# Kernel tuning notes

Hardware: AMD Instinct MI355X
Metric: run time of the kernel (lower is better)

The kernel has to match this reference:

```python
import jax, jax.numpy as jnp
import numpy as np

D_MODEL = 1024
NUM_HEADS = 16
D_HEAD = D_MODEL // NUM_HEADS
MAX_DISTANCE = 128
SEQ_LEN = 2048


def setup_inputs() -> dict:
    key = jax.random.key(0)
    k_x, k_qkv, k_out, k_bias = jax.random.split(key, 4)
    scale = 1.0 / np.sqrt(D_MODEL)
    return {
        "x": jax.random.normal(k_x, (SEQ_LEN, D_MODEL), dtype=jnp.float32),
        "w_qkv": jax.random.normal(k_qkv, (D_MODEL, 3 * D_MODEL), dtype=jnp.float32) * scale,
        "w_out": jax.random.normal(k_out, (D_MODEL, D_MODEL), dtype=jnp.float32) * scale,
        "rel_bias": jax.random.normal(k_bias, (MAX_DISTANCE, NUM_HEADS), dtype=jnp.float32) * 0.02,
    }


def _position_bias(rel_bias, seq_len):
    # relative_position[q, k] = k - q; bucket = clip(|rel|, 0, max_distance-1)
    ctx = jnp.arange(seq_len)[:, None]
    mem = jnp.arange(seq_len)[None, :]
    bucket = jnp.clip(jnp.abs(mem - ctx), 0, MAX_DISTANCE - 1)  # [q, k]
    return rel_bias[bucket]  # [q, k, h]


def reference(x, w_qkv, w_out, rel_bias):
    seq_len = x.shape[0]
    qkv = x @ w_qkv  # [s, 3*d_model]
    q, k, v = jnp.split(qkv, 3, axis=-1)
    q = q.reshape(seq_len, NUM_HEADS, D_HEAD)
    k = k.reshape(seq_len, NUM_HEADS, D_HEAD)
    v = v.reshape(seq_len, NUM_HEADS, D_HEAD)
    bias = _position_bias(rel_bias, seq_len)  # [q, k, h]
    # flax dot_product_attention semantics: scale q by 1/sqrt(d_head), add bias, softmax over kv
    scores = jnp.einsum("qhd,khd->hqk", q, k) / jnp.sqrt(jnp.asarray(D_HEAD, q.dtype))
    scores = scores + jnp.transpose(bias, (2, 0, 1))  # [h, q, k]
    weights = jax.nn.softmax(scores, axis=-1)
    attn = jnp.einsum("hqk,khd->qhd", weights, v)  # [s, h, d_head]
    attn = attn.reshape(1, seq_len, D_MODEL)
    return attn @ w_out  # [1, s, d_model]
```

## Files before the change

### kernel.cpp

```cpp
#include <hip/hip_runtime.h>
#include <hip/hip_bf16.h>

#define SEQ   2048
#define DM    1024
#define NH    16
#define DH    64
#define MAXD  128

typedef __attribute__((ext_vector_type(8))) short  short8;
typedef __attribute__((ext_vector_type(4))) float  float4v;

__device__ __forceinline__ short8 ld8(const void* p) {
    short8 v; __builtin_memcpy(&v, p, 16); return v;
}
__device__ __forceinline__ void st8(void* p, short8 v) {
    __builtin_memcpy(p, &v, 16);
}
__device__ __forceinline__ short bf16bits(float f) {
    __hip_bfloat16 b = __float2bfloat16(f);
    short s; __builtin_memcpy(&s, &b, 2); return s;
}
__device__ __forceinline__ float bits2f(short s) {
    unsigned u = (unsigned)(unsigned short)s << 16;
    return __builtin_bit_cast(float, u);
}

__device__ __forceinline__ void async16(void* lds, const void* g) {
    __builtin_amdgcn_global_load_lds(
        (const __attribute__((address_space(1))) unsigned int*)g,
        (__attribute__((address_space(3))) unsigned int*)lds, 16, 0, 0);
}

template <int CTRL>
__device__ __forceinline__ float dppmov(float x) {
    return __builtin_bit_cast(float,
        __builtin_amdgcn_update_dpp(0, __builtin_bit_cast(int, x), CTRL, 0xf, 0xf, true));
}
__device__ __forceinline__ float red16max(float x) {
    x = fmaxf(x, dppmov<0xB1>(x));
    x = fmaxf(x, dppmov<0x4E>(x));
    x = fmaxf(x, dppmov<0x141>(x));
    x = fmaxf(x, dppmov<0x140>(x));
    return x;
}
__device__ __forceinline__ float red16sum(float x) {
    x += dppmov<0xB1>(x);
    x += dppmov<0x4E>(x);
    x += dppmov<0x141>(x);
    x += dppmov<0x140>(x);
    return x;
}

__global__ __launch_bounds__(256) void cvt_f32_bf16(
    const float* __restrict__ src, __hip_bfloat16* __restrict__ dst) {
    const size_t i = ((size_t)blockIdx.x * 256 + threadIdx.x) * 8;
    float f[8]; __builtin_memcpy(f, src + i, 32);
    short8 v;
#pragma unroll
    for (int j = 0; j < 8; ++j) v[j] = bf16bits(f[j]);
    st8(dst + i, v);
}

__global__ __launch_bounds__(256) void transpose_weights(
    const float* __restrict__ wq, const float* __restrict__ wo,
    __hip_bfloat16* __restrict__ wqT, __hip_bfloat16* __restrict__ woT) {
    __shared__ __hip_bfloat16 tile[32][33];
    const int t = threadIdx.x;
    const int tx = t % 32, ty = t / 32;
    const int bx = blockIdx.x, r0 = blockIdx.y * 32;
    const float* src; __hip_bfloat16* dst; int ss, ds, c0;
    if (bx < 96) { src = wq; dst = wqT; ss = 3 * DM; ds = DM; c0 = bx * 32; }
    else         { src = wo; dst = woT; ss = DM;     ds = DM; c0 = (bx - 96) * 32; }
#pragma unroll
    for (int i = 0; i < 4; ++i)
        tile[ty + i * 8][tx] = __float2bfloat16(src[(size_t)(r0 + ty + i * 8) * ss + c0 + tx]);
    __syncthreads();
#pragma unroll
    for (int i = 0; i < 4; ++i)
        dst[(size_t)(c0 + ty + i * 8) * ds + r0 + tx] = tile[tx][ty + i * 8];
}

__global__ __launch_bounds__(256) void transpose_v(
    const __hip_bfloat16* __restrict__ src, __hip_bfloat16* __restrict__ dst,
    int s_stride, int d_stride) {
    __shared__ __hip_bfloat16 tile[32][33];
    const int t = threadIdx.x;
    const int tx = t % 32, ty = t / 32;
    const int c0 = blockIdx.x * 32, r0 = blockIdx.y * 32;
#pragma unroll
    for (int i = 0; i < 4; ++i)
        tile[ty + i * 8][tx] = src[(size_t)(r0 + ty + i * 8) * s_stride + c0 + tx];
    __syncthreads();
#pragma unroll
    for (int i = 0; i < 4; ++i)
        dst[(size_t)(c0 + ty + i * 8) * d_stride + r0 + tx] = tile[tx][ty + i * 8];
}

template <int NT, typename TC>
__global__ __launch_bounds__(256) void gemm_mfma(
    const __hip_bfloat16* __restrict__ A,
    const __hip_bfloat16* __restrict__ BT,
    TC* __restrict__ C,
    int M, int N, int K) {
    __shared__ short As[128 * 32];
    __shared__ short Bs[32 * NT * 32];

    const int t = threadIdx.x;
    const int w = t >> 6, lane = t & 63;
    const int l15 = lane & 15, quad = lane >> 4;
    const int row0 = blockIdx.y * 128;
    const int col0 = blockIdx.x * (32 * NT);
    const int wm = w >> 1, wn = w & 1;

    float4v acc[4][NT];
#pragma unroll
    for (int i = 0; i < 4; ++i)
#pragma unroll
        for (int j = 0; j < NT; ++j) acc[i][j] = (float4v){0.f, 0.f, 0.f, 0.f};

    const int mloc0 = lane >> 2;
    const int u     = lane & 3;

    for (int k0 = 0; k0 < K; k0 += 32) {
#pragma unroll
        for (int i = 0; i < 2; ++i) {
            const int c = 2 * w + i;
            async16(&As[c * 512], A + (size_t)(row0 + c * 16 + mloc0) * K + k0 + u * 8);
        }
#pragma unroll
        for (int i = 0; i < NT / 2; ++i) {
            const int c = (NT / 2) * w + i;
            async16(&Bs[c * 512], BT + (size_t)(col0 + c * 16 + mloc0) * K + k0 + u * 8);
        }
        __syncthreads();

        short8 af[4], bf[NT];
#pragma unroll
        for (int mt = 0; mt < 4; ++mt)
            af[mt] = ld8(&As[(wm * 64 + mt * 16 + l15) * 32 + quad * 8]);
#pragma unroll
        for (int nt = 0; nt < NT; ++nt)
            bf[nt] = ld8(&Bs[(wn * 16 * NT + nt * 16 + l15) * 32 + quad * 8]);
#pragma unroll
        for (int mt = 0; mt < 4; ++mt)
#pragma unroll
            for (int nt = 0; nt < NT; ++nt)
                acc[mt][nt] = __builtin_amdgcn_mfma_f32_16x16x32_bf16(
                    af[mt], bf[nt], acc[mt][nt], 0, 0, 0);
        __syncthreads();
    }

#pragma unroll
    for (int mt = 0; mt < 4; ++mt)
#pragma unroll
        for (int nt = 0; nt < NT; ++nt)
#pragma unroll
            for (int r = 0; r < 4; ++r) {
                const int row = row0 + wm * 64 + mt * 16 + quad * 4 + r;
                const int col = col0 + wn * 16 * NT + nt * 16 + l15;
                float v = acc[mt][nt][r];
                if constexpr (__is_same(TC, float)) C[(size_t)row * N + col] = v;
                else C[(size_t)row * N + col] = __float2bfloat16(v);
            }
}

#define TK  128
#define KS  68
#define VS  136

__global__ __launch_bounds__(256) void attn_mfma(
    const __hip_bfloat16* __restrict__ qkv,
    const __hip_bfloat16* __restrict__ vT,
    const float* __restrict__ rel_bias,
    __hip_bfloat16* __restrict__ attnb) {
    __shared__ short Kt[TK * KS];
    __shared__ short Vt[DH * VS];
    __shared__ short Pl[4 * 16 * VS];
    __shared__ float biasL[MAXD];

    const int t = threadIdx.x;
    const int w = t >> 6, lane = t & 63;
    const int l15 = lane & 15, quad = lane >> 4;
    const int h  = blockIdx.y;
    const int q0 = blockIdx.x * 64;
    const int qw = q0 + w * 16;

    if (t < MAXD) biasL[t] = rel_bias[t * NH + h];

    short8 qf[2];
#pragma unroll
    for (int c = 0; c < 2; ++c) {
        short8 raw = ld8(qkv + (size_t)(qw + l15) * (3 * DM) + h * DH + c * 32 + quad * 8);
#pragma unroll
        for (int j = 0; j < 8; ++j) qf[c][j] = bf16bits(bits2f(raw[j]) * 0.125f);
    }

    float4v o_acc[4];
#pragma unroll
    for (int nt = 0; nt < 4; ++nt) o_acc[nt] = (float4v){0.f, 0.f, 0.f, 0.f};
    float m_i[4], l_i[4];
#pragma unroll
    for (int r = 0; r < 4; ++r) { m_i[r] = -1e30f; l_i[r] = 0.f; }

    for (int kb = 0; kb < SEQ / TK; ++kb) {
        const int k0 = kb * TK;
#pragma unroll
        for (int p = 0; p < 4; ++p) {
            const int idx = p * 256 + t;
            const int row = idx >> 3, u = idx & 7;
            st8(&Kt[row * KS + u * 8],
                ld8(qkv + (size_t)(k0 + row) * (3 * DM) + DM + h * DH + u * 8));
        }
#pragma unroll
        for (int p = 0; p < 4; ++p) {
            const int idx = p * 256 + t;
            const int row = idx >> 4, u = idx & 15;
            st8(&Vt[row * VS + u * 8],
                ld8(vT + (size_t)(h * DH + row) * SEQ + k0 + u * 8));
        }
        __syncthreads();

        float4v s_acc[8];
#pragma unroll
        for (int kt = 0; kt < 8; ++kt) s_acc[kt] = (float4v){0.f, 0.f, 0.f, 0.f};
#pragma unroll
        for (int c = 0; c < 2; ++c)
#pragma unroll
            for (int kt = 0; kt < 8; ++kt) {
                short8 kf = ld8(&Kt[(kt * 16 + l15) * KS + (c * 4 + quad) * 8]);
                s_acc[kt] = __builtin_amdgcn_mfma_f32_16x16x32_bf16(qf[c], kf, s_acc[kt], 0, 0, 0);
            }

        float sv[8][4];
        const int dlo = k0 - (qw + 15);
        const int dhi = qw - (k0 + TK - 1);
        if (dlo >= MAXD - 1 || dhi >= MAXD - 1) {
            const float bu = biasL[MAXD - 1];
#pragma unroll
            for (int kt = 0; kt < 8; ++kt)
#pragma unroll
                for (int r = 0; r < 4; ++r) sv[kt][r] = s_acc[kt][r] + bu;
        } else {
#pragma unroll
            for (int kt = 0; kt < 8; ++kt)
#pragma unroll
                for (int r = 0; r < 4; ++r) {
                    const int kg = k0 + kt * 16 + l15;
                    const int qg = qw + quad * 4 + r;
                    int rel = kg - qg; if (rel < 0) rel = -rel;
                    if (rel > MAXD - 1) rel = MAXD - 1;
                    sv[kt][r] = s_acc[kt][r] + biasL[rel];
                }
        }

        float rowm[4];
#pragma unroll
        for (int r = 0; r < 4; ++r) {
            float m = sv[0][r];
#pragma unroll
            for (int kt = 1; kt < 8; ++kt) m = fmaxf(m, sv[kt][r]);
            rowm[r] = red16max(m);
        }

        float al[4], rs[4];
#pragma unroll
        for (int r = 0; r < 4; ++r) {
            const float mn = fmaxf(m_i[r], rowm[r]);
            al[r] = __expf(m_i[r] - mn);
            m_i[r] = mn;
            rs[r] = 0.f;
        }
#pragma unroll
        for (int kt = 0; kt < 8; ++kt)
#pragma unroll
            for (int r = 0; r < 4; ++r) {
                const float p = __expf(sv[kt][r] - m_i[r]);
                sv[kt][r] = p;
                rs[r] += p;
            }
#pragma unroll
        for (int r = 0; r < 4; ++r) {
            rs[r] = red16sum(rs[r]);
            l_i[r] = l_i[r] * al[r] + rs[r];
        }
#pragma unroll
        for (int nt = 0; nt < 4; ++nt)
#pragma unroll
            for (int r = 0; r < 4; ++r) o_acc[nt][r] *= al[r];

#pragma unroll
        for (int kt = 0; kt < 8; ++kt)
#pragma unroll
            for (int r = 0; r < 4; ++r)
                Pl[w * 16 * VS + (quad * 4 + r) * VS + kt * 16 + l15] = bf16bits(sv[kt][r]);

#pragma unroll
        for (int kc = 0; kc < 4; ++kc) {
            short8 pf = ld8(&Pl[w * 16 * VS + l15 * VS + kc * 32 + quad * 8]);
#pragma unroll
            for (int nt = 0; nt < 4; ++nt) {
                short8 vf = ld8(&Vt[(nt * 16 + l15) * VS + kc * 32 + quad * 8]);
                o_acc[nt] = __builtin_amdgcn_mfma_f32_16x16x32_bf16(pf, vf, o_acc[nt], 0, 0, 0);
            }
        }
        __syncthreads();
    }

#pragma unroll
    for (int nt = 0; nt < 4; ++nt)
#pragma unroll
        for (int r = 0; r < 4; ++r) {
            const int row = qw + quad * 4 + r;
            const int col = h * DH + nt * 16 + l15;
            attnb[(size_t)row * DM + col] = __float2bfloat16(o_acc[nt][r] / l_i[r]);
        }
}

extern "C" void kernel_launch(void* const* d_in, const int* in_sizes, int n_in,
                              void* d_out, int out_size, void* d_ws, size_t ws_size,
                              hipStream_t stream) {
    const float* x        = (const float*)d_in[0];
    const float* w_qkv    = (const float*)d_in[1];
    const float* w_out    = (const float*)d_in[2];
    const float* rel_bias = (const float*)d_in[3];
    float* out = (float*)d_out;

    char* p = (char*)d_ws;
    __hip_bfloat16* xb    = (__hip_bfloat16*)p;  p += (size_t)SEQ * DM * 2;
    __hip_bfloat16* wqT   = (__hip_bfloat16*)p;  p += (size_t)3 * DM * DM * 2;
    __hip_bfloat16* woT   = (__hip_bfloat16*)p;  p += (size_t)DM * DM * 2;
    __hip_bfloat16* qkvb  = (__hip_bfloat16*)p;  p += (size_t)SEQ * 3 * DM * 2;
    __hip_bfloat16* vT    = (__hip_bfloat16*)p;  p += (size_t)DM * SEQ * 2;
    __hip_bfloat16* attnb = (__hip_bfloat16*)p;

    cvt_f32_bf16<<<SEQ * DM / (256 * 8), 256, 0, stream>>>(x, xb);

    transpose_weights<<<dim3(128, 32), 256, 0, stream>>>(w_qkv, w_out, wqT, woT);

    gemm_mfma<4, __hip_bfloat16><<<dim3(3 * DM / 128, SEQ / 128), 256, 0, stream>>>(
        xb, wqT, qkvb, SEQ, 3 * DM, DM);

    transpose_v<<<dim3(DM / 32, SEQ / 32), 256, 0, stream>>>(
        qkvb + 2 * DM, vT, 3 * DM, SEQ);

    attn_mfma<<<dim3(SEQ / 64, NH), 256, 0, stream>>>(qkvb, vT, rel_bias, attnb);

    gemm_mfma<2, float><<<dim3(DM / 64, SEQ / 128), 256, 0, stream>>>(
        attnb, woT, out, SEQ, DM, DM);
}
```

Measured before the change: 177.7 us.

## Merge prep kernels, shrink GEMM tiles, add 64x64 output GEMM, tweak V padding

Folds the x-to-bf16 conversion into the weight-transpose kernel as extra blocks, which removes one launch. Halves the QKV GEMM column tile so more blocks are launched. Adds a dedicated 64x64-tile GEMM for the output projection so that launch also has more blocks. Changes the V LDS stride padding from 136 to 132. Smaller tiles give more parallelism across CUs but less data reuse per block, and the new stride can change LDS bank conflicts.

```diff
diff --git a/kernel.cpp b/kernel.cpp
--- a/kernel.cpp
+++ b/kernel.cpp
@@ -51,23 +51,26 @@
     return x;
 }
 
-__global__ __launch_bounds__(256) void cvt_f32_bf16(
-    const float* __restrict__ src, __hip_bfloat16* __restrict__ dst) {
-    const size_t i = ((size_t)blockIdx.x * 256 + threadIdx.x) * 8;
-    float f[8]; __builtin_memcpy(f, src + i, 32);
-    short8 v;
-#pragma unroll
-    for (int j = 0; j < 8; ++j) v[j] = bf16bits(f[j]);
-    st8(dst + i, v);
-}
-
-__global__ __launch_bounds__(256) void transpose_weights(
+__global__ __launch_bounds__(256) void prep_kernel(
     const float* __restrict__ wq, const float* __restrict__ wo,
-    __hip_bfloat16* __restrict__ wqT, __hip_bfloat16* __restrict__ woT) {
+    const float* __restrict__ x,
+    __hip_bfloat16* __restrict__ wqT, __hip_bfloat16* __restrict__ woT,
+    __hip_bfloat16* __restrict__ xb) {
+    const int t = threadIdx.x;
+    const int bx = blockIdx.x;
+    if (bx >= 128) {
+        const size_t id = (size_t)(bx - 128) * 32 + blockIdx.y;
+        const size_t i  = id * 2048 + t * 8;
+        float f[8]; __builtin_memcpy(f, x + i, 32);
+        short8 v;
+#pragma unroll
+        for (int j = 0; j < 8; ++j) v[j] = bf16bits(f[j]);
+        st8(xb + i, v);
+        return;
+    }
     __shared__ __hip_bfloat16 tile[32][33];
-    const int t = threadIdx.x;
     const int tx = t % 32, ty = t / 32;
-    const int bx = blockIdx.x, r0 = blockIdx.y * 32;
+    const int r0 = blockIdx.y * 32;
     const float* src; __hip_bfloat16* dst; int ss, ds, c0;
     if (bx < 96) { src = wq; dst = wqT; ss = 3 * DM; ds = DM; c0 = bx * 32; }
     else         { src = wo; dst = woT; ss = DM;     ds = DM; c0 = (bx - 96) * 32; }
@@ -164,9 +167,66 @@
             }
 }
 
+__global__ __launch_bounds__(256) void gemm64(
+    const __hip_bfloat16* __restrict__ A,
+    const __hip_bfloat16* __restrict__ BT,
+    float* __restrict__ C,
+    int M, int N, int K) {
+    __shared__ short As[64 * 32];
+    __shared__ short Bs[64 * 32];
+
+    const int t = threadIdx.x;
+    const int w = t >> 6, lane = t & 63;
+    const int l15 = lane & 15, quad = lane >> 4;
+    const int row0 = blockIdx.y * 64;
+    const int col0 = blockIdx.x * 64;
+    const int wm = w >> 1, wn = w & 1;
+
+    float4v acc[2][2];
+#pragma unroll
+    for (int i = 0; i < 2; ++i)
+#pragma unroll
+        for (int j = 0; j < 2; ++j) acc[i][j] = (float4v){0.f, 0.f, 0.f, 0.f};
+
+    const int mloc0 = lane >> 2;
+    const int u     = lane & 3;
+
+    for (int k0 = 0; k0 < K; k0 += 32) {
+        async16(&As[w * 512], A  + (size_t)(row0 + w * 16 + mloc0) * K + k0 + u * 8);
+        async16(&Bs[w * 512], BT + (size_t)(col0 + w * 16 + mloc0) * K + k0 + u * 8);
+        __syncthreads();
+
+        short8 af[2], bf[2];
+#pragma unroll
+        for (int mt = 0; mt < 2; ++mt)
+            af[mt] = ld8(&As[(wm * 32 + mt * 16 + l15) * 32 + quad * 8]);
+#pragma unroll
+        for (int nt = 0; nt < 2; ++nt)
+            bf[nt] = ld8(&Bs[(wn * 32 + nt * 16 + l15) * 32 + quad * 8]);
+#pragma unroll
+        for (int mt = 0; mt < 2; ++mt)
+#pragma unroll
+            for (int nt = 0; nt < 2; ++nt)
+                acc[mt][nt] = __builtin_amdgcn_mfma_f32_16x16x32_bf16(
+                    af[mt], bf[nt], acc[mt][nt], 0, 0, 0);
+        __syncthreads();
+    }
+
+#pragma unroll
+    for (int mt = 0; mt < 2; ++mt)
+#pragma unroll
+        for (int nt = 0; nt < 2; ++nt)
+#pragma unroll
+            for (int r = 0; r < 4; ++r) {
+                const int row = row0 + wm * 32 + mt * 16 + quad * 4 + r;
+                const int col = col0 + wn * 32 + nt * 16 + l15;
+                C[(size_t)row * N + col] = acc[mt][nt][r];
+            }
+}
+
 #define TK  128
 #define KS  68
-#define VS  136
+#define VS  132
 
 __global__ __launch_bounds__(256) void attn_mfma(
     const __hip_bfloat16* __restrict__ qkv,
@@ -333,11 +393,9 @@
     __hip_bfloat16* vT    = (__hip_bfloat16*)p;  p += (size_t)DM * SEQ * 2;
     __hip_bfloat16* attnb = (__hip_bfloat16*)p;
 
-    cvt_f32_bf16<<<SEQ * DM / (256 * 8), 256, 0, stream>>>(x, xb);
-
-    transpose_weights<<<dim3(128, 32), 256, 0, stream>>>(w_qkv, w_out, wqT, woT);
-
-    gemm_mfma<4, __hip_bfloat16><<<dim3(3 * DM / 128, SEQ / 128), 256, 0, stream>>>(
+    prep_kernel<<<dim3(160, 32), 256, 0, stream>>>(w_qkv, w_out, x, wqT, woT, xb);
+
+    gemm_mfma<2, __hip_bfloat16><<<dim3(3 * DM / 64, SEQ / 128), 256, 0, stream>>>(
         xb, wqT, qkvb, SEQ, 3 * DM, DM);
 
     transpose_v<<<dim3(DM / 32, SEQ / 32), 256, 0, stream>>>(
@@ -345,6 +403,6 @@
 
     attn_mfma<<<dim3(SEQ / 64, NH), 256, 0, stream>>>(qkvb, vT, rel_bias, attnb);
 
-    gemm_mfma<2, float><<<dim3(DM / 64, SEQ / 128), 256, 0, stream>>>(
+    gemm64<<<dim3(DM / 64, SEQ / 64), 256, 0, stream>>>(
         attnb, woT, out, SEQ, DM, DM);
 }
```

After: 169.7 us. 4.5% less time.
